# Kernel optimization log

Measured on AMD Instinct MI355X. Metric: run time of the kernel, lower is better.

## Reference

```python
import jax, jax.numpy as jnp
import numpy as np

B, T, SD, CD = 2048, 512, 8, 8
H = 64 + SD  # control_rnn_size + state_dim = 72


def setup_inputs() -> dict:
    key = jax.random.key(0)
    ks = jax.random.split(key, 16)
    s = 0.05
    inp = {
        "x": jax.random.normal(ks[0], (B, SD), jnp.float32),
        "rnn_input": jax.random.normal(ks[1], (B, T, CD + 1), jnp.float32),
        "deltas": jax.random.uniform(ks[2], (B, T, 1), jnp.float32),
        "h_lens": jax.random.randint(ks[3], (B,), T // 2, T + 1, jnp.int32),
        "W_ih": s * jax.random.normal(ks[4], (4 * H, CD + 1), jnp.float32),
        "W_hh": s * jax.random.normal(ks[5], (4 * H, H), jnp.float32),
        "b_ih": jnp.zeros((4 * H,), jnp.float32),
        "b_hh": jnp.zeros((4 * H,), jnp.float32),
        "enc_W1": s * jax.random.normal(ks[6], (256, SD), jnp.float32),
        "enc_b1": jnp.zeros((256,), jnp.float32),
        "enc_W2": s * jax.random.normal(ks[7], (256, 256), jnp.float32),
        "enc_b2": jnp.zeros((256,), jnp.float32),
        "enc_W3": s * jax.random.normal(ks[8], (64, 256), jnp.float32),
        "enc_b3": jnp.zeros((64,), jnp.float32),
        "dec_W1": s * jax.random.normal(ks[9], (288, H), jnp.float32),
        "dec_b1": jnp.zeros((288,), jnp.float32),
        "dec_W2": s * jax.random.normal(ks[10], (288, 288), jnp.float32),
        "dec_b2": jnp.zeros((288,), jnp.float32),
        "dec_W3": s * jax.random.normal(ks[11], (SD, 288), jnp.float32),
        "dec_b3": jnp.zeros((SD,), jnp.float32),
    }
    return inp


def _mlp(z, Ws_bs):
    # Linear->Tanh repeated, final Linear without activation
    *hidden, (Wf, bf) = Ws_bs
    for W, b in hidden:
        z = jnp.tanh(z @ W.T + b)
    return z @ Wf.T + bf


def _lstm(rnn_input, h0, c0, W_ih, W_hh, b_ih, b_hh):
    # rnn_input: [B,T,I]; h0,c0: [B,H]. PyTorch gate order: i,f,g,o.
    x_proj = rnn_input @ W_ih.T + (b_ih + b_hh)  # [B,T,4H]

    def step(carry, xt):
        h, c = carry
        gates = xt + h @ W_hh.T
        i, f, g, o = jnp.split(gates, 4, axis=-1)
        i, f, o = jax.nn.sigmoid(i), jax.nn.sigmoid(f), jax.nn.sigmoid(o)
        c = f * c + i * jnp.tanh(g)
        h = o * jnp.tanh(c)
        return (h, c), h

    _, hs = jax.lax.scan(step, (h0, c0), jnp.swapaxes(x_proj, 0, 1))
    return jnp.swapaxes(hs, 0, 1)  # [B,T,H]


def reference(x, rnn_input, deltas, h_lens, W_ih, W_hh, b_ih, b_hh,
              enc_W1, enc_b1, enc_W2, enc_b2, enc_W3, enc_b3,
              dec_W1, dec_b1, dec_W2, dec_b2, dec_W3, dec_b3):
    h0 = _mlp(x, [(enc_W1, enc_b1), (enc_W2, enc_b2), (enc_W3, enc_b3)])  # [B,64]
    h0_stack = jnp.concatenate([x, h0], axis=1)  # [B,H]
    c0 = jnp.zeros_like(h0_stack)
    h = _lstm(rnn_input, h0_stack, c0, W_ih, W_hh, b_ih, b_hh)  # [B,T,H]
    # roll by 1 with h0 in slot 0
    h_shift = jnp.concatenate([h0_stack[:, None, :], h[:, :-1, :]], axis=1)
    encoded = (1.0 - deltas) * h_shift + deltas * h  # [B,T,H]
    dec_in = encoded[jnp.arange(encoded.shape[0]), h_lens - 1, :]  # [B,H]
    out = _mlp(dec_in, [(dec_W1, dec_b1), (dec_W2, dec_b2), (dec_W3, dec_b3)])
    return out[:, :SD]
```

## Files before the change

### kernel.cpp

```cpp
#include <hip/hip_runtime.h>
#include <cstdint>

#define HH 72
#define NR 8
#define NTH 576
#define NBLK 256
#define TT 512

typedef __attribute__((ext_vector_type(8))) _Float16 half8;
typedef __attribute__((ext_vector_type(4))) float f32x4;

#if __has_builtin(__builtin_amdgcn_exp2f)
#define EXP2(x) __builtin_amdgcn_exp2f(x)
#else
#define EXP2(x) exp2f(x)
#endif
#if __has_builtin(__builtin_amdgcn_rcpf)
#define RCP(x) __builtin_amdgcn_rcpf(x)
#else
#define RCP(x) (1.0f/(x))
#endif

__device__ __forceinline__ float fsig(float x) {
  float e = EXP2(x * -1.442695040888963f);
  return RCP(1.0f + e);
}
__device__ __forceinline__ float ftanh(float x) {
  float e = EXP2(x * -2.885390081777927f);
  return fmaf(2.0f, RCP(1.0f + e), -1.0f);
}

__device__ __forceinline__ unsigned short f2h(float v) {
  union { _Float16 h; unsigned short u; } cv;
  cv.h = (_Float16)v;
  return cv.u;
}

__device__ __forceinline__ int bidx(int k, int m) {
  return ((k >> 5)*4 + ((k >> 3) & 3))*64 + m*8 + (k & 7);
}

__device__ __forceinline__ float cellUpd(float ig, float fg, float gg, float og, float& c) {
  c = fmaf(fsig(fg), c, fsig(ig)*ftanh(gg));
  return fsig(og)*ftanh(c);
}

#define FMA4(A, W_, P_) { \
  const float4 _fa = *(const float4*)(P_); \
  A[0] = fmaf((W_), _fa.x, A[0]); A[1] = fmaf((W_), _fa.y, A[1]); \
  A[2] = fmaf((W_), _fa.z, A[2]); A[3] = fmaf((W_), _fa.w, A[3]); }

__global__ void cfm_sort(const int* __restrict__ h_lens, int* __restrict__ perm) {
  __shared__ int hist[257];
  __shared__ int offs[257];
  const int t = threadIdx.x;
  for (int i = t; i < 257; i += 256) hist[i] = 0;
  __syncthreads();
  for (int i = t; i < 2048; i += 256) {
    int bkt = min(max(h_lens[i] - 256, 0), 256);
    atomicAdd(&hist[bkt], 1);
  }
  __syncthreads();
  if (t == 0) { int s = 0; for (int i = 0; i < 257; ++i) { offs[i] = s; s += hist[i]; } }
  __syncthreads();
  for (int i = t; i < 2048; i += 256) {
    int bkt = min(max(h_lens[i] - 256, 0), 256);
    int pos = atomicAdd(&offs[bkt], 1);
    perm[pos] = i;
  }
}

__global__ __launch_bounds__(NTH, 2)
void cfm_main(const float* __restrict__ x, const float* __restrict__ rnn,
              const float* __restrict__ deltas, const int* __restrict__ h_lens,
              const float* __restrict__ W_ih, const float* __restrict__ W_hh,
              const float* __restrict__ b_ih, const float* __restrict__ b_hh,
              const float* __restrict__ eW1, const float* __restrict__ eb1,
              const float* __restrict__ eW2, const float* __restrict__ eb2,
              const float* __restrict__ eW3, const float* __restrict__ eb3,
              const float* __restrict__ dW1, const float* __restrict__ db1,
              const float* __restrict__ dW2, const float* __restrict__ db2,
              const float* __restrict__ dW3, const float* __restrict__ db3,
              const int* __restrict__ perm, float* __restrict__ out)
{
  __shared__ __align__(16) unsigned short hF[2][768];
  __shared__ __align__(16) float gS[2304];
  __shared__ __align__(16) float rnnS[2336];
  __shared__ __align__(16) float snapP[NR][HH];
  __shared__ __align__(16) float snapC[NR][HH];
  __shared__ __align__(16) float hS[HH*NR];
  __shared__ __align__(16) float xS[8*NR];
  __shared__ int brS[NR];
  __shared__ int idxS[NR];
  __shared__ float dS[NR];

  const int t  = threadIdx.x;
  const int bb = blockIdx.x;

  for (int i = t; i < 768; i += NTH) ((unsigned*)hF)[i] = 0;

  if (t < NR) {
    int row = perm ? perm[bb*NR + t] : (bb*NR + t);
    brS[t]  = row;
    idxS[t] = h_lens[row] - 1;
  }
  __syncthreads();

  int maxIdx = idxS[0];
  #pragma unroll
  for (int r = 1; r < NR; ++r) maxIdx = max(maxIdx, idxS[r]);

  const int lane = t & 63;
  const int wv   = t >> 6;
  const int col  = lane & 15;
  const int q_a  = lane >> 4;
  const int cL   = col & 7;
  const int gHi  = col >> 3;
  const int uA   = 4*(2*wv + gHi) + q_a;
  const int cidxE  = idxS[cL];
  const int cidxm1 = cidxE - 1;
  const int ibA  = bidx(uA, cL);
  const int bOff0 = (0*4 + q_a)*64 + cL*8;
  const int bOff1 = (1*4 + q_a)*64 + cL*8;
  const int bOff2 = (2*4 + q_a)*64 + cL*8;
  float cstA = 0.f;

  const int pfR = t / 72;
  const int pfP = t - pfR*72;
  const float4* rnnRow = (const float4*)(rnn + (size_t)brS[pfR]*4608) + pfP;
  float4 pf = rnnRow[0];

  const bool doXt = (t < 72);
  int xtDst = 0, xtSrc = 0;
  if (doXt) {
    int rX = t / 9, kX = t - rX*9;
    xtDst = bidx(72 + kX, rX);
    xtSrc = rX*292 + kX;
  }

  if (t < 64) { int r = t >> 3, k = t & 7; xS[k*8 + r] = x[brS[r]*8 + k]; }
  __syncthreads();

  float* z1S = gS;
  if (t < 512) {
    int n = t >> 1, rh = (t & 1)*4;
    float acc[4];
    float b = eb1[n];
    acc[0]=b; acc[1]=b; acc[2]=b; acc[3]=b;
    #pragma unroll
    for (int k = 0; k < 8; ++k) { float w = eW1[n*8 + k]; FMA4(acc, w, &xS[k*8 + rh]); }
    #pragma unroll
    for (int j = 0; j < 4; ++j) z1S[n*8 + rh + j] = ftanh(acc[j]);
  }
  __syncthreads();
  float* z2S = rnnS;
  if (t < 512) {
    int n = t >> 1, rh = (t & 1)*4;
    float acc[4];
    float b = eb2[n];
    acc[0]=b; acc[1]=b; acc[2]=b; acc[3]=b;
    const float4* w4 = (const float4*)(eW2 + n*256);
    #pragma unroll 4
    for (int k4 = 0; k4 < 64; ++k4) {
      float4 w = w4[k4];
      FMA4(acc, w.x, &z1S[(4*k4+0)*8 + rh]);
      FMA4(acc, w.y, &z1S[(4*k4+1)*8 + rh]);
      FMA4(acc, w.z, &z1S[(4*k4+2)*8 + rh]);
      FMA4(acc, w.w, &z1S[(4*k4+3)*8 + rh]);
    }
    #pragma unroll
    for (int j = 0; j < 4; ++j) z2S[n*8 + rh + j] = ftanh(acc[j]);
  }
  __syncthreads();
  if (t < 128) {
    int o = t >> 1, rh = (t & 1)*4;
    float acc[4];
    float b = eb3[o];
    acc[0]=b; acc[1]=b; acc[2]=b; acc[3]=b;
    const float4* w4 = (const float4*)(eW3 + o*256);
    #pragma unroll 4
    for (int k4 = 0; k4 < 64; ++k4) {
      float4 w = w4[k4];
      FMA4(acc, w.x, &z2S[(4*k4+0)*8 + rh]);
      FMA4(acc, w.y, &z2S[(4*k4+1)*8 + rh]);
      FMA4(acc, w.z, &z2S[(4*k4+2)*8 + rh]);
      FMA4(acc, w.w, &z2S[(4*k4+3)*8 + rh]);
    }
    #pragma unroll
    for (int j = 0; j < 4; ++j) hF[0][bidx(8 + o, rh + j)] = f2h(acc[j]);
  } else if (t < 192) {
    int tt2 = t - 128; int r = tt2 >> 3, k = tt2 & 7;
    hF[0][bidx(k, r)] = f2h(xS[k*8 + r]);
  }

  half8 Af[2][3];
  f32x4 biasq[2];
  #pragma unroll
  for (int i = 0; i < 2; ++i) {
    int u = 4*(2*wv + i) + q_a;
    biasq[i].x = b_ih[u]       + b_hh[u];
    biasq[i].y = b_ih[72 + u]  + b_hh[72 + u];
    biasq[i].z = b_ih[144 + u] + b_hh[144 + u];
    biasq[i].w = b_ih[216 + u] + b_hh[216 + u];
    int nprime = (2*wv + i)*16 + col;
    int srcrow = (nprime & 3)*72 + (nprime >> 2);
    #pragma unroll
    for (int kt = 0; kt < 3; ++kt) {
      union { unsigned short u16[8]; half8 h; } cw;
      #pragma unroll
      for (int j = 0; j < 8; ++j) {
        int k = kt*32 + q_a*8 + j;
        float v = 0.f;
        if (k < 72)      v = W_hh[srcrow*HH + k];
        else if (k < 81) v = W_ih[srcrow*9 + (k - 72)];
        cw.u16[j] = f2h(v);
      }
      Af[i][kt] = cw.h;
    }
  }

#define STEP(PAR) { \
    const unsigned short* hb = &hF[PAR][0]; \
    unsigned short* hn = &hF[(PAR) ^ 1][0]; \
    half8 bf0 = *(const half8*)(hb + bOff0); \
    half8 bf1 = *(const half8*)(hb + bOff1); \
    half8 bf2 = *(const half8*)(hb + bOff2); \
    f32x4 a0 = __builtin_amdgcn_mfma_f32_16x16x32_f16(Af[0][0], bf0, biasq[0], 0, 0, 0); \
    f32x4 a1 = __builtin_amdgcn_mfma_f32_16x16x32_f16(Af[1][0], bf0, biasq[1], 0, 0, 0); \
    a0 = __builtin_amdgcn_mfma_f32_16x16x32_f16(Af[0][1], bf1, a0, 0, 0, 0); \
    a1 = __builtin_amdgcn_mfma_f32_16x16x32_f16(Af[1][1], bf1, a1, 0, 0, 0); \
    a0 = __builtin_amdgcn_mfma_f32_16x16x32_f16(Af[0][2], bf2, a0, 0, 0, 0); \
    a1 = __builtin_amdgcn_mfma_f32_16x16x32_f16(Af[1][2], bf2, a1, 0, 0, 0); \
    float ig = gHi ? a1.x : a0.x; \
    float fg = gHi ? a1.y : a0.y; \
    float gg = gHi ? a1.z : a0.z; \
    float og = gHi ? a1.w : a0.w; \
    float hv = cellUpd(ig, fg, gg, og, cstA); \
    hn[ibA] = f2h(hv); \
    if (step == cidxm1) snapP[cL][uA] = hv; \
    if (step == cidxE)  snapC[cL][uA] = hv; \
    if (doXt && tc < 31) hn[xtDst] = f2h(rnnS[xtSrc + (tc + 1)*9]); \
    __syncthreads(); \
    ++tc; ++step; }

  int step = 0;
  for (int chunk = 0; chunk*32 <= maxIdx; ++chunk) {
    __syncthreads();
    *(float4*)&rnnS[pfR*292 + pfP*4] = pf;
    if ((chunk + 1)*32 <= maxIdx) pf = rnnRow[(chunk + 1)*72];
    __syncthreads();
    if (doXt) hF[0][xtDst] = f2h(rnnS[xtSrc]);
    __syncthreads();
    const int lim = min(31, maxIdx - chunk*32);
    int tc = 0;
    while (tc + 1 <= lim) { STEP(0) STEP(1) }
    if (tc <= lim) { STEP(0) }
  }
#undef STEP

  if (t < NR) dS[t] = deltas[brS[t]*TT + idxS[t]];
  __syncthreads();

  {
    int u = t % 72, r = t / 72;
    float d = dS[r];
    float sp = snapP[r][u], sc = snapC[r][u];
    hS[u*8 + r] = fmaf(d, sc - sp, sp);
  }
  __syncthreads();

  float* d1S = rnnS;
  {
    int n = t >> 1, rh = (t & 1)*4;
    float acc[4];
    float b = db1[n];
    acc[0]=b; acc[1]=b; acc[2]=b; acc[3]=b;
    const float4* w4 = (const float4*)(dW1 + n*HH);
    #pragma unroll 2
    for (int k4 = 0; k4 < 18; ++k4) {
      float4 w = w4[k4];
      FMA4(acc, w.x, &hS[(4*k4+0)*8 + rh]);
      FMA4(acc, w.y, &hS[(4*k4+1)*8 + rh]);
      FMA4(acc, w.z, &hS[(4*k4+2)*8 + rh]);
      FMA4(acc, w.w, &hS[(4*k4+3)*8 + rh]);
    }
    #pragma unroll
    for (int j = 0; j < 4; ++j) d1S[n*8 + rh + j] = ftanh(acc[j]);
  }
  __syncthreads();

  float* d2S = gS;
  {
    int n = t >> 1, rh = (t & 1)*4;
    float acc[4];
    float b = db2[n];
    acc[0]=b; acc[1]=b; acc[2]=b; acc[3]=b;
    const float4* w4 = (const float4*)(dW2 + n*288);
    #pragma unroll 4
    for (int k4 = 0; k4 < 72; ++k4) {
      float4 w = w4[k4];
      FMA4(acc, w.x, &d1S[(4*k4+0)*8 + rh]);
      FMA4(acc, w.y, &d1S[(4*k4+1)*8 + rh]);
      FMA4(acc, w.z, &d1S[(4*k4+2)*8 + rh]);
      FMA4(acc, w.w, &d1S[(4*k4+3)*8 + rh]);
    }
    #pragma unroll
    for (int j = 0; j < 4; ++j) d2S[n*8 + rh + j] = ftanh(acc[j]);
  }
  __syncthreads();

  if (t < 64) {
    int o = t & 7, r = t >> 3;
    float acc3 = db3[o];
    const float* wr = dW3 + o*288;
    #pragma unroll 4
    for (int k = 0; k < 288; ++k) acc3 = fmaf(wr[k], d2S[k*8 + r], acc3);
    out[brS[r]*8 + o] = acc3;
  }
}

extern "C" void kernel_launch(void* const* d_in, const int* in_sizes, int n_in,
                              void* d_out, int out_size, void* d_ws, size_t ws_size,
                              hipStream_t stream) {
  const float* x      = (const float*)d_in[0];
  const float* rnn    = (const float*)d_in[1];
  const float* deltas = (const float*)d_in[2];
  const int*   h_lens = (const int*)  d_in[3];
  const float* W_ih   = (const float*)d_in[4];
  const float* W_hh   = (const float*)d_in[5];
  const float* b_ih   = (const float*)d_in[6];
  const float* b_hh   = (const float*)d_in[7];
  const float* eW1    = (const float*)d_in[8];
  const float* eb1    = (const float*)d_in[9];
  const float* eW2    = (const float*)d_in[10];
  const float* eb2    = (const float*)d_in[11];
  const float* eW3    = (const float*)d_in[12];
  const float* eb3    = (const float*)d_in[13];
  const float* dW1    = (const float*)d_in[14];
  const float* db1    = (const float*)d_in[15];
  const float* dW2    = (const float*)d_in[16];
  const float* db2    = (const float*)d_in[17];
  const float* dW3    = (const float*)d_in[18];
  const float* db3    = (const float*)d_in[19];
  float* out = (float*)d_out;

  int* perm = nullptr;
  if (ws_size >= 2048 * sizeof(int)) {
    perm = (int*)d_ws;
    cfm_sort<<<1, 256, 0, stream>>>(h_lens, perm);
  }
  cfm_main<<<NBLK, NTH, 0, stream>>>(x, rnn, deltas, h_lens, W_ih, W_hh, b_ih, b_hh,
                                     eW1, eb1, eW2, eb2, eW3, eb3,
                                     dW1, db1, dW2, db2, dW3, db3,
                                     perm, out);
}
```

Before: 355.6 us.

## Stage per-chunk inputs in a separate buffer and shorten the recurrent MFMA dependency chain

The per-step input slice is now written once per 32-step chunk into a dedicated hXT buffer. The third K-tile B operand is read from that buffer (or from a zero pad) instead of being written into the recurrent h buffer every step. The MFMA chain is split into two independent accumulations that are added at the end, which shortens the serial dependency per step. Snapshot stores become register selects written once after the loop, and __syncthreads is replaced by a raw lgkmcnt wait plus s_barrier. The cost is a larger LDS footprint and an inline-asm barrier that relies on correct wait semantics.

```diff
diff --git a/kernel.cpp b/kernel.cpp
--- a/kernel.cpp
+++ b/kernel.cpp
@@ -20,6 +20,8 @@
 #else
 #define RCP(x) (1.0f/(x))
 #endif
+
+#define BARL() asm volatile("s_waitcnt lgkmcnt(0)\n\ts_barrier" ::: "memory")
 
 __device__ __forceinline__ float fsig(float x) {
   float e = EXP2(x * -1.442695040888963f);
@@ -83,7 +85,9 @@
               const float* __restrict__ dW3, const float* __restrict__ db3,
               const int* __restrict__ perm, float* __restrict__ out)
 {
-  __shared__ __align__(16) unsigned short hF[2][768];
+  __shared__ __align__(16) unsigned short hF[2][576];
+  __shared__ __align__(16) unsigned short hXT[32*128];
+  __shared__ __align__(16) unsigned short zPadS[64];
   __shared__ __align__(16) float gS[2304];
   __shared__ __align__(16) float rnnS[2336];
   __shared__ __align__(16) float snapP[NR][HH];
@@ -97,7 +101,8 @@
   const int t  = threadIdx.x;
   const int bb = blockIdx.x;
 
-  for (int i = t; i < 768; i += NTH) ((unsigned*)hF)[i] = 0;
+  for (int i = t; i < 2048; i += NTH) ((unsigned*)hXT)[i] = 0;
+  if (t < 32) ((unsigned*)zPadS)[t] = 0;
 
   if (t < NR) {
     int row = perm ? perm[bb*NR + t] : (bb*NR + t);
@@ -120,23 +125,17 @@
   const int cidxE  = idxS[cL];
   const int cidxm1 = cidxE - 1;
   const int ibA  = bidx(uA, cL);
-  const int bOff0 = (0*4 + q_a)*64 + cL*8;
-  const int bOff1 = (1*4 + q_a)*64 + cL*8;
-  const int bOff2 = (2*4 + q_a)*64 + cL*8;
+  const int c8   = cL*8;
+  const int bOff0 = (0*4 + q_a)*64 + c8;
+  const int bOff1 = (1*4 + q_a)*64 + c8;
+  const int midOff = (q_a - 1)*64 + c8;
   float cstA = 0.f;
+  float hvP = 0.f, hvC = 0.f;
 
   const int pfR = t / 72;
   const int pfP = t - pfR*72;
   const float4* rnnRow = (const float4*)(rnn + (size_t)brS[pfR]*4608) + pfP;
   float4 pf = rnnRow[0];
-
-  const bool doXt = (t < 72);
-  int xtDst = 0, xtSrc = 0;
-  if (doXt) {
-    int rX = t / 9, kX = t - rX*9;
-    xtDst = bidx(72 + kX, rX);
-    xtSrc = rX*292 + kX;
-  }
 
   if (t < 64) { int r = t >> 3, k = t & 7; xS[k*8 + r] = x[brS[r]*8 + k]; }
   __syncthreads();
@@ -219,45 +218,57 @@
     }
   }
 
+#define MFMA16(A, B, C) __builtin_amdgcn_mfma_f32_16x16x32_f16(A, B, C, 0, 0, 0)
+  const f32x4 zero4 = {0.f, 0.f, 0.f, 0.f};
 #define STEP(PAR) { \
     const unsigned short* hb = &hF[PAR][0]; \
     unsigned short* hn = &hF[(PAR) ^ 1][0]; \
+    const unsigned short* p2 = (q_a == 0) ? (hb + 512 + c8) \
+                             : (q_a == 3) ? (&zPadS[0] + c8) \
+                             : (&hXT[0] + tc*128 + midOff); \
     half8 bf0 = *(const half8*)(hb + bOff0); \
     half8 bf1 = *(const half8*)(hb + bOff1); \
-    half8 bf2 = *(const half8*)(hb + bOff2); \
-    f32x4 a0 = __builtin_amdgcn_mfma_f32_16x16x32_f16(Af[0][0], bf0, biasq[0], 0, 0, 0); \
-    f32x4 a1 = __builtin_amdgcn_mfma_f32_16x16x32_f16(Af[1][0], bf0, biasq[1], 0, 0, 0); \
-    a0 = __builtin_amdgcn_mfma_f32_16x16x32_f16(Af[0][1], bf1, a0, 0, 0, 0); \
-    a1 = __builtin_amdgcn_mfma_f32_16x16x32_f16(Af[1][1], bf1, a1, 0, 0, 0); \
-    a0 = __builtin_amdgcn_mfma_f32_16x16x32_f16(Af[0][2], bf2, a0, 0, 0, 0); \
-    a1 = __builtin_amdgcn_mfma_f32_16x16x32_f16(Af[1][2], bf2, a1, 0, 0, 0); \
-    float ig = gHi ? a1.x : a0.x; \
-    float fg = gHi ? a1.y : a0.y; \
-    float gg = gHi ? a1.z : a0.z; \
-    float og = gHi ? a1.w : a0.w; \
+    half8 bf2 = *(const half8*)p2; \
+    f32x4 y0 = MFMA16(Af[0][1], bf1, zero4); \
+    f32x4 y1 = MFMA16(Af[1][1], bf1, zero4); \
+    f32x4 x0 = MFMA16(Af[0][0], bf0, biasq[0]); \
+    f32x4 x1 = MFMA16(Af[1][0], bf0, biasq[1]); \
+    x0 = MFMA16(Af[0][2], bf2, x0); \
+    x1 = MFMA16(Af[1][2], bf2, x1); \
+    f32x4 a0 = x0 + y0; \
+    f32x4 a1 = x1 + y1; \
+    float ig = gHi ? a1.x : a0.x, fg = gHi ? a1.y : a0.y; \
+    float gg = gHi ? a1.z : a0.z, og = gHi ? a1.w : a0.w; \
     float hv = cellUpd(ig, fg, gg, og, cstA); \
     hn[ibA] = f2h(hv); \
-    if (step == cidxm1) snapP[cL][uA] = hv; \
-    if (step == cidxE)  snapC[cL][uA] = hv; \
-    if (doXt && tc < 31) hn[xtDst] = f2h(rnnS[xtSrc + (tc + 1)*9]); \
-    __syncthreads(); \
+    hvP = (step == cidxm1) ? hv : hvP; \
+    hvC = (step == cidxE)  ? hv : hvC; \
+    BARL(); \
     ++tc; ++step; }
 
   int step = 0;
   for (int chunk = 0; chunk*32 <= maxIdx; ++chunk) {
-    __syncthreads();
+    BARL();
     *(float4*)&rnnS[pfR*292 + pfP*4] = pf;
     if ((chunk + 1)*32 <= maxIdx) pf = rnnRow[(chunk + 1)*72];
-    __syncthreads();
-    if (doXt) hF[0][xtDst] = f2h(rnnS[xtSrc]);
-    __syncthreads();
+    BARL();
+    for (int e = t; e < 2304; e += NTH) {
+      int r = e / 288, rem = e - r*288;
+      int tcs = rem / 9, kk = rem - tcs*9;
+      float v = rnnS[r*292 + tcs*9 + kk];
+      int dst = tcs*128 + ((kk < 8) ? (r*8 + kk) : (64 + r*8));
+      hXT[dst] = f2h(v);
+    }
+    BARL();
     const int lim = min(31, maxIdx - chunk*32);
     int tc = 0;
     while (tc + 1 <= lim) { STEP(0) STEP(1) }
     if (tc <= lim) { STEP(0) }
   }
 #undef STEP
-
+#undef MFMA16
+
+  snapP[cL][uA] = hvP;  snapC[cL][uA] = hvC;
   if (t < NR) dS[t] = deltas[brS[t]*TT + idxS[t]];
   __syncthreads();
 
```

After: 399.7 us. 1.12x slower.
